# Performance work log

Measured on AMD Instinct MI355X. Metric: run time of the kernel, lower is better.

## Reference

```python
import jax, jax.numpy as jnp
import numpy as np

DIM = 128
HEADS = 4
NS = 7          # neighborhood_size (odd)
RADIUS = NS // 2
EXP = 2         # ffn expansion
EPS = 1e-8


def rmsnorm(x, w):
    # x: [B,C,H,W], w: [1,C,1,1]
    rms = jnp.mean(jnp.square(x), axis=1, keepdims=True)
    return x * jax.lax.rsqrt(rms + EPS) * w


def conv1x1(x, w, b):
    # w: [Cout,Cin], b: [Cout]
    return jnp.einsum('oi,bihw->bohw', w, x) + b[None, :, None, None]


def setup_inputs() -> dict:
    key = jax.random.key(0)
    ks = jax.random.split(key, 20)
    B, C, H, W = 2, DIM, 64, 64
    s = 0.02
    d = {
        'z': jax.random.normal(ks[0], (B, C, H, W), jnp.float32),
        'h': jax.random.normal(ks[1], (B, C, H, W), jnp.float32),
        'wz_norm': jnp.ones((1, C, 1, 1), jnp.float32),
        'wh_norm': jnp.ones((1, C, 1, 1), jnp.float32),
        'wq': jax.random.normal(ks[2], (C, C), jnp.float32) * s,
        'bq': jnp.zeros((C,), jnp.float32),
        'wk': jax.random.normal(ks[3], (C, C), jnp.float32) * s,
        'bk': jnp.zeros((C,), jnp.float32),
        'wv': jax.random.normal(ks[4], (C, C), jnp.float32) * s,
        'bv': jnp.zeros((C,), jnp.float32),
        'wo': jax.random.normal(ks[5], (C, C), jnp.float32) * s,
        'bo': jnp.zeros((C,), jnp.float32),
        'wffn_norm': jnp.ones((1, C, 1, 1), jnp.float32),
        'w1': jax.random.normal(ks[6], (C * EXP, C), jnp.float32) * s,
        'b1': jnp.zeros((C * EXP,), jnp.float32),
        'w2': jax.random.normal(ks[7], (C, C * EXP), jnp.float32) * s,
        'b2': jnp.zeros((C,), jnp.float32),
    }
    return d


def neighborhood_cross_attn(zq, hk, wq, bq, wk, bk, wv, bv, wo, bo):
    B, C, H, W = zq.shape
    hd = C // HEADS
    scale = hd ** (-0.5)
    q = conv1x1(zq, wq, bq)
    k = conv1x1(hk, wk, bk)
    v = conv1x1(hk, wv, bv)
    # [B, heads, H, W, hd]
    qh = q.reshape(B, HEADS, hd, H, W).transpose(0, 1, 3, 4, 2)
    kh = k.reshape(B, HEADS, hd, H, W).transpose(0, 1, 3, 4, 2)
    vh = v.reshape(B, HEADS, hd, H, W).transpose(0, 1, 3, 4, 2)
    offs = jnp.arange(-RADIUS, RADIUS + 1)
    dy, dx = jnp.meshgrid(offs, offs, indexing='ij')
    dy = dy.reshape(-1)  # [K]
    dx = dx.reshape(-1)
    by, bx = jnp.meshgrid(jnp.arange(H), jnp.arange(W), indexing='ij')
    ny = by[:, :, None] + dy  # [H, W, K]
    nx = bx[:, :, None] + dx
    valid = (ny >= 0) & (ny < H) & (nx >= 0) & (nx < W)
    nyc = jnp.clip(ny, 0, H - 1)
    nxc = jnp.clip(nx, 0, W - 1)
    # gather neighbors: [B, heads, H, W, K, hd]
    k_nb = kh[:, :, nyc, nxc]
    v_nb = vh[:, :, nyc, nxc]
    attn = jnp.einsum('bnhwd,bnhwkd->bnhwk', qh, k_nb) * scale
    attn = jnp.where(valid[None, None], attn, jnp.finfo(attn.dtype).min)
    p = jax.nn.softmax(attn, axis=-1)
    out = jnp.einsum('bnhwk,bnhwkd->bnhwd', p, v_nb)
    out = out.transpose(0, 1, 4, 2, 3).reshape(B, C, H, W)
    return conv1x1(out, wo, bo)


def reference(z, h, wz_norm, wh_norm, wq, bq, wk, bk, wv, bv, wo, bo,
              wffn_norm, w1, b1, w2, b2):
    h_norm = rmsnorm(h, wh_norm)
    z_norm = rmsnorm(z, wz_norm)
    z = z + neighborhood_cross_attn(z_norm, h_norm, wq, bq, wk, bk, wv, bv, wo, bo)
    y = rmsnorm(z, wffn_norm)
    y = conv1x1(y, w1, b1)
    y = jax.nn.gelu(y, approximate=False)
    y = conv1x1(y, w2, b2)
    return z + y
```

## Files before the change

kernel.cpp:

```cpp
#include <hip/hip_runtime.h>
#include <math.h>

#define CDIM 128
#define HW   4096
#define HEADS 4
#define HD   32

typedef __attribute__((ext_vector_type(8))) short bf16x8;
typedef __attribute__((ext_vector_type(4))) float f32x4;

static __device__ __forceinline__ unsigned int f2bf(float f) {
  union { float f; unsigned int u; } v; v.f = f;
  unsigned int r = v.u + 0x7FFF + ((v.u >> 16) & 1);
  return r >> 16;
}
static __device__ __forceinline__ float bflo(unsigned int u) {
  return __uint_as_float(u << 16);
}
static __device__ __forceinline__ float bfhi(unsigned int u) {
  return __uint_as_float(u & 0xFFFF0000u);
}
static __device__ __forceinline__ float gelu_f(float v) {
  float y = v * (1.595769122f + 0.071354816f * v * v);
  return v / (1.0f + __expf(-y));
}

__global__ __launch_bounds__(256) void head(
    const float* __restrict__ z, const float* __restrict__ h,
    const float* __restrict__ wzn, const float* __restrict__ whn,
    const float* __restrict__ wq, const float* __restrict__ bq,
    const float* __restrict__ wk, const float* __restrict__ bk,
    const float* __restrict__ wv, const float* __restrict__ bv,
    const float* __restrict__ wo, const float* __restrict__ w1,
    const float* __restrict__ w2, ushort* __restrict__ WB,
    ushort* __restrict__ Qb, ushort* __restrict__ Kb, ushort* __restrict__ Vb) {
  const int sel = blockIdx.y, t = threadIdx.x;
  if (sel == 3) {
    int e = (blockIdx.x * 256 + t) * 4;
    if (e < 81920) {
      const float* src; int off;
      if      (e < 16384) { src = wo; off = 0; }
      else if (e < 49152) { src = w1; off = 16384; }
      else                { src = w2; off = 49152; }
      float4 v = *(const float4*)&src[e - off];
      uint2 r;
      r.x = f2bf(v.x) | (f2bf(v.y) << 16);
      r.y = f2bf(v.z) | (f2bf(v.w) << 16);
      *(uint2*)&WB[49152 + e] = r;
    }
    return;
  }
  __shared__ __align__(16) ushort sW[128 * 128];
  __shared__ __align__(16) ushort sX[64 * 128];
  __shared__ float sh[4][64];

  const float* X    = (sel == 0) ? z : h;
  const float* wn   = (sel == 0) ? wzn : whn;
  const float* Wf   = (sel == 0) ? wq : (sel == 1 ? wk : wv);
  const float* bias = (sel == 0) ? bq : (sel == 1 ? bk : bv);
  ushort* outB      = (sel == 0) ? Qb : (sel == 1 ? Kb : Vb);

#pragma unroll
  for (int i = 0; i < 8; ++i) {
    int u  = t + i * 256;
    int o  = u >> 4;
    int k8 = (u & 15) * 8;
    float4 v0 = *(const float4*)&Wf[o * 128 + k8];
    float4 v1 = *(const float4*)&Wf[o * 128 + k8 + 4];
    uint4 pk;
    pk.x = f2bf(v0.x) | (f2bf(v0.y) << 16);
    pk.y = f2bf(v0.z) | (f2bf(v0.w) << 16);
    pk.z = f2bf(v1.x) | (f2bf(v1.y) << 16);
    pk.w = f2bf(v1.z) | (f2bf(v1.w) << 16);
    int idx = (o * 128 + k8) ^ ((o & 7) << 3);
    *(uint4*)&sW[idx] = pk;
  }

  const int pl = t & 63, g = t >> 6;
  const int gp = blockIdx.x * 64 + pl;
  const size_t xbase = (size_t)(gp >> 12) * CDIM * HW + (gp & 4095);
  float vals[32];
  float ss = 0.f;
#pragma unroll
  for (int j = 0; j < 32; ++j) {
    float v = X[xbase + (size_t)(g * 32 + j) * HW];
    vals[j] = v;
    ss += v * v;
  }
  sh[g][pl] = ss;
  __syncthreads();
  float tot = sh[0][pl] + sh[1][pl] + sh[2][pl] + sh[3][pl];
  float inv = rsqrtf(tot * (1.0f / CDIM) + 1e-8f);
#pragma unroll
  for (int jj = 0; jj < 4; ++jj) {
    unsigned int u[4];
#pragma unroll
    for (int p2 = 0; p2 < 4; ++p2) {
      int j = jj * 8 + p2 * 2;
      float a = vals[j]     * inv * wn[g * 32 + j];
      float b = vals[j + 1] * inv * wn[g * 32 + j + 1];
      u[p2] = f2bf(a) | (f2bf(b) << 16);
    }
    int idx = (pl * 128 + g * 32 + jj * 8) ^ ((pl & 7) << 3);
    *(uint4*)&sX[idx] = make_uint4(u[0], u[1], u[2], u[3]);
  }
  __syncthreads();

  const int w = t >> 6, l = t & 63, lr = l & 15, lk = l >> 4;
  const int m0 = w * 32;
  const int swz = (lr & 7) << 3;
  f32x4 acc[2][4] = {};
#pragma unroll
  for (int k0 = 0; k0 < 128; k0 += 32) {
    bf16x8 a0 = *(const bf16x8*)&sW[((m0 + lr) * 128 + k0 + lk * 8) ^ swz];
    bf16x8 a1 = *(const bf16x8*)&sW[((m0 + 16 + lr) * 128 + k0 + lk * 8) ^ swz];
    bf16x8 b[4];
#pragma unroll
    for (int nf = 0; nf < 4; ++nf)
      b[nf] = *(const bf16x8*)&sX[((nf * 16 + lr) * 128 + k0 + lk * 8) ^ swz];
#pragma unroll
    for (int nf = 0; nf < 4; ++nf) {
      acc[0][nf] = __builtin_amdgcn_mfma_f32_16x16x32_bf16(a0, b[nf], acc[0][nf], 0, 0, 0);
      acc[1][nf] = __builtin_amdgcn_mfma_f32_16x16x32_bf16(a1, b[nf], acc[1][nf], 0, 0, 0);
    }
  }
#pragma unroll
  for (int mf = 0; mf < 2; ++mf) {
    int obase = m0 + mf * 16 + lk * 4;
    f32x4 bv = *(const f32x4*)&bias[obase];
#pragma unroll
    for (int nf = 0; nf < 4; ++nf) {
      int P = blockIdx.x * 64 + nf * 16 + lr;
      uint2 pk;
      pk.x = f2bf(acc[mf][nf][0] + bv[0]) | (f2bf(acc[mf][nf][1] + bv[1]) << 16);
      pk.y = f2bf(acc[mf][nf][2] + bv[2]) | (f2bf(acc[mf][nf][3] + bv[3]) << 16);
      *(uint2*)&outB[(size_t)P * CDIM + obase] = pk;
    }
  }
}

__global__ __launch_bounds__(512) void nattn(
    const ushort* __restrict__ Q, const ushort* __restrict__ K,
    const ushort* __restrict__ V, ushort* __restrict__ ATT) {
  __shared__ __align__(16) unsigned int smem[20480];
  float* sS = (float*)smem;
  const int t  = threadIdx.x;
  const int px = t & 127;
  const int x  = px & 63;
  const int r  = px >> 6;
  const int dg = t >> 7;
  const int y0 = blockIdx.x * 2;
  const int h  = blockIdx.y;
  const int b  = blockIdx.z;
  const int ybase = y0 - 3;

  {
    int yy = t >> 6, xs = t & 63;
    int gy = min(max(ybase + yy, 0), 63);
    size_t gb = ((size_t)(b * HW + gy * 64 + xs)) * 64 + h * 16;
    const unsigned int* Ku = (const unsigned int*)K;
    const unsigned int* Vu = (const unsigned int*)V;
    int lb = (yy * 64 + xs) * 20;
#pragma unroll
    for (int i = 0; i < 4; ++i) {
      uint4 kv = *(const uint4*)&Ku[gb + i * 4];
      uint4 vv = *(const uint4*)&Vu[gb + i * 4];
      *(uint4*)&smem[lb + i * 4]         = kv;
      *(uint4*)&smem[10240 + lb + i * 4] = vv;
    }
  }
  const int Pq = b * HW + (y0 + r) * 64 + x;
  const unsigned int* Qu = (const unsigned int*)Q;
  float q[32];
#pragma unroll
  for (int i = 0; i < 4; ++i) {
    uint4 u4 = *(const uint4*)&Qu[(size_t)Pq * 64 + h * 16 + i * 4];
    q[i*8+0] = bflo(u4.x); q[i*8+1] = bfhi(u4.x);
    q[i*8+2] = bflo(u4.y); q[i*8+3] = bfhi(u4.y);
    q[i*8+4] = bflo(u4.z); q[i*8+5] = bfhi(u4.z);
    q[i*8+6] = bflo(u4.w); q[i*8+7] = bfhi(u4.w);
  }
  __syncthreads();

  const float scale = 0.17677669529663687f;
  const int nb0    = (dg == 0) ? 0 : dg * 12 + 1;
  const int ncount = (dg == 0) ? 13 : 12;
  float sreg[13];
#pragma unroll
  for (int j = 0; j < 13; ++j) {
    if (j < ncount) {
      int nb = nb0 + j;
      int dy = nb / 7 - 3;
      int dx = nb % 7 - 3;
      int ry = r + dy + 3;
      int nx = x + dx;
      int xx = min(max(nx, 0), 63);
      int ny = y0 + r + dy;
      bool valid = (ny >= 0) && (ny <= 63) && (nx >= 0) && (nx <= 63);
      const unsigned int* kb = &smem[(ry * 64 + xx) * 20];
      float acc = 0.f;
#pragma unroll
      for (int c = 0; c < 4; ++c) {
        uint4 u4 = *(const uint4*)&kb[c * 4];
        acc += q[c*8+0] * bflo(u4.x) + q[c*8+1] * bfhi(u4.x);
        acc += q[c*8+2] * bflo(u4.y) + q[c*8+3] * bfhi(u4.y);
        acc += q[c*8+4] * bflo(u4.z) + q[c*8+5] * bfhi(u4.z);
        acc += q[c*8+6] * bflo(u4.w) + q[c*8+7] * bfhi(u4.w);
      }
      sreg[j] = valid ? __expf(acc * scale - 8.0f) : 0.0f;
    }
  }
  __syncthreads();
#pragma unroll
  for (int j = 0; j < 13; ++j)
    if (j < ncount) sS[(nb0 + j) * 128 + px] = sreg[j];
  __syncthreads();

  float o[8] = {0.f, 0.f, 0.f, 0.f, 0.f, 0.f, 0.f, 0.f};
  float sum = 0.f;
#pragma unroll
  for (int nb = 0; nb < 49; ++nb) {
    float p = sS[nb * 128 + px];
    sum += p;
    int ry = r + nb / 7;
    int xx = min(max(x + nb % 7 - 3, 0), 63);
    uint4 u4 = *(const uint4*)&smem[10240 + (ry * 64 + xx) * 20 + dg * 4];
    o[0] += p * bflo(u4.x); o[1] += p * bfhi(u4.x);
    o[2] += p * bflo(u4.y); o[3] += p * bfhi(u4.y);
    o[4] += p * bflo(u4.z); o[5] += p * bfhi(u4.z);
    o[6] += p * bflo(u4.w); o[7] += p * bfhi(u4.w);
  }
  float inv = 1.0f / sum;
  unsigned int pk[4];
#pragma unroll
  for (int j = 0; j < 4; ++j)
    pk[j] = f2bf(o[2*j] * inv) | (f2bf(o[2*j+1] * inv) << 16);
  *(uint4*)&ATT[(size_t)Pq * CDIM + h * HD + dg * 8] = make_uint4(pk[0], pk[1], pk[2], pk[3]);
}

__global__ __launch_bounds__(256) void tail(
    const ushort* __restrict__ ATT, const ushort* __restrict__ WB,
    const float* __restrict__ bo, const float* __restrict__ z,
    const float* __restrict__ wfn, const float* __restrict__ b1,
    const float* __restrict__ b2, float* __restrict__ out) {
  __shared__ __align__(16) float  zlds[32][132];
  __shared__ __align__(16) ushort fn_s[32 * 128];
  __shared__ __align__(16) ushort hid_s[32 * 256];
  __shared__ float sums[32][17];
  __shared__ float sinv[32];
  const ushort* Wo = WB + 49152;
  const ushort* W1 = WB + 65536;
  const ushort* W2 = WB + 98304;
  const int t = threadIdx.x, w = t >> 6, l = t & 63, lr = l & 15, lk = l >> 4;
  const int pblk = blockIdx.x * 32;
  const int m0 = w * 32;

  {
    const ushort* A0 = Wo + (size_t)(m0 + lr) * 128 + lk * 8;
    const ushort* A1 = A0 + 16 * 128;
    const ushort* B0 = ATT + (size_t)(pblk + lr) * 128 + lk * 8;
    const ushort* B1 = B0 + 16 * 128;
    f32x4 acc[2][2] = {};
#pragma unroll
    for (int k0 = 0; k0 < 128; k0 += 32) {
      bf16x8 a0 = *(const bf16x8*)(A0 + k0);
      bf16x8 a1 = *(const bf16x8*)(A1 + k0);
      bf16x8 b0 = *(const bf16x8*)(B0 + k0);
      bf16x8 b1 = *(const bf16x8*)(B1 + k0);
      acc[0][0] = __builtin_amdgcn_mfma_f32_16x16x32_bf16(a0, b0, acc[0][0], 0, 0, 0);
      acc[0][1] = __builtin_amdgcn_mfma_f32_16x16x32_bf16(a0, b1, acc[0][1], 0, 0, 0);
      acc[1][0] = __builtin_amdgcn_mfma_f32_16x16x32_bf16(a1, b0, acc[1][0], 0, 0, 0);
      acc[1][1] = __builtin_amdgcn_mfma_f32_16x16x32_bf16(a1, b1, acc[1][1], 0, 0, 0);
    }
#pragma unroll
    for (int nf = 0; nf < 2; ++nf) {
      int px = nf * 16 + lr;
      int P  = pblk + px;
      int b_ = P >> 12, p = P & 4095;
      float ss = 0.f;
#pragma unroll
      for (int mf = 0; mf < 2; ++mf) {
        int row0 = m0 + mf * 16 + lk * 4;
        f32x4 bv = *(const f32x4*)&bo[row0];
        f32x4 rr;
#pragma unroll
        for (int j = 0; j < 4; ++j) {
          size_t gi = ((size_t)(b_ * CDIM + row0 + j)) * HW + p;
          float u = acc[mf][nf][j] + bv[j] + z[gi];
          rr[j] = u;
          ss += u * u;
        }
        *(f32x4*)&zlds[px][row0] = rr;
      }
      sums[px][w * 4 + lk] = ss;
    }
  }
  __syncthreads();
  if (t < 32) {
    float tot = 0.f;
#pragma unroll
    for (int i = 0; i < 16; ++i) tot += sums[t][i];
    sinv[t] = rsqrtf(tot * (1.0f / CDIM) + 1e-8f);
  }
  __syncthreads();
#pragma unroll
  for (int nf = 0; nf < 2; ++nf) {
    int px = nf * 16 + lr;
    float inv = sinv[px];
#pragma unroll
    for (int mf = 0; mf < 2; ++mf) {
      int row0 = m0 + mf * 16 + lk * 4;
      f32x4 uu = *(const f32x4*)&zlds[px][row0];
      f32x4 wf = *(const f32x4*)&wfn[row0];
      uint2 pk;
      pk.x = f2bf(uu[0] * inv * wf[0]) | (f2bf(uu[1] * inv * wf[1]) << 16);
      pk.y = f2bf(uu[2] * inv * wf[2]) | (f2bf(uu[3] * inv * wf[3]) << 16);
      int idx = (px * 128 + row0) ^ ((px & 7) << 3);
      *(uint2*)&fn_s[idx] = pk;
    }
  }
  __syncthreads();
  {
    const int hm0 = w * 64;
    const ushort* A0 = W1 + (size_t)(hm0 + lr) * 128 + lk * 8;
    f32x4 acc1[4][2] = {};
#pragma unroll
    for (int k0 = 0; k0 < 128; k0 += 32) {
      bf16x8 a[4], b[2];
#pragma unroll
      for (int mf = 0; mf < 4; ++mf) a[mf] = *(const bf16x8*)(A0 + mf * 16 * 128 + k0);
#pragma unroll
      for (int nf = 0; nf < 2; ++nf) {
        int px = nf * 16 + lr;
        b[nf] = *(const bf16x8*)&fn_s[(px * 128 + k0 + lk * 8) ^ ((px & 7) << 3)];
      }
#pragma unroll
      for (int mf = 0; mf < 4; ++mf)
#pragma unroll
        for (int nf = 0; nf < 2; ++nf)
          acc1[mf][nf] = __builtin_amdgcn_mfma_f32_16x16x32_bf16(a[mf], b[nf], acc1[mf][nf], 0, 0, 0);
    }
#pragma unroll
    for (int mf = 0; mf < 4; ++mf) {
      int ch0 = hm0 + mf * 16 + lk * 4;
      f32x4 bv = *(const f32x4*)&b1[ch0];
#pragma unroll
      for (int nf = 0; nf < 2; ++nf) {
        int px = nf * 16 + lr;
        float v0 = gelu_f(acc1[mf][nf][0] + bv[0]);
        float v1 = gelu_f(acc1[mf][nf][1] + bv[1]);
        float v2 = gelu_f(acc1[mf][nf][2] + bv[2]);
        float v3 = gelu_f(acc1[mf][nf][3] + bv[3]);
        uint2 pk;
        pk.x = f2bf(v0) | (f2bf(v1) << 16);
        pk.y = f2bf(v2) | (f2bf(v3) << 16);
        int idx = (px * 256 + ch0) ^ ((px & 7) << 3);
        *(uint2*)&hid_s[idx] = pk;
      }
    }
  }
  __syncthreads();
  {
    const ushort* C0 = W2 + (size_t)(m0 + lr) * 256 + lk * 8;
    f32x4 acc2[2][2] = {};
#pragma unroll
    for (int k0 = 0; k0 < 256; k0 += 32) {
      bf16x8 a0 = *(const bf16x8*)(C0 + k0);
      bf16x8 a1 = *(const bf16x8*)(C0 + 16 * 256 + k0);
      bf16x8 b[2];
#pragma unroll
      for (int nf = 0; nf < 2; ++nf) {
        int px = nf * 16 + lr;
        b[nf] = *(const bf16x8*)&hid_s[(px * 256 + k0 + lk * 8) ^ ((px & 7) << 3)];
      }
      acc2[0][0] = __builtin_amdgcn_mfma_f32_16x16x32_bf16(a0, b[0], acc2[0][0], 0, 0, 0);
      acc2[0][1] = __builtin_amdgcn_mfma_f32_16x16x32_bf16(a0, b[1], acc2[0][1], 0, 0, 0);
      acc2[1][0] = __builtin_amdgcn_mfma_f32_16x16x32_bf16(a1, b[0], acc2[1][0], 0, 0, 0);
      acc2[1][1] = __builtin_amdgcn_mfma_f32_16x16x32_bf16(a1, b[1], acc2[1][1], 0, 0, 0);
    }
#pragma unroll
    for (int mf = 0; mf < 2; ++mf) {
      int row0 = m0 + mf * 16 + lk * 4;
      f32x4 bv = *(const f32x4*)&b2[row0];
#pragma unroll
      for (int nf = 0; nf < 2; ++nf) {
        int px = nf * 16 + lr;
        int P  = pblk + px;
        int b_ = P >> 12, p = P & 4095;
        f32x4 zz = *(const f32x4*)&zlds[px][row0];
#pragma unroll
        for (int j = 0; j < 4; ++j) {
          size_t gi = ((size_t)(b_ * CDIM + row0 + j)) * HW + p;
          out[gi] = acc2[mf][nf][j] + bv[j] + zz[j];
        }
      }
    }
  }
}

extern "C" void kernel_launch(void* const* d_in, const int* in_sizes, int n_in,
                              void* d_out, int out_size, void* d_ws, size_t ws_size,
                              hipStream_t stream) {
  const float* z   = (const float*)d_in[0];
  const float* h   = (const float*)d_in[1];
  const float* wzn = (const float*)d_in[2];
  const float* whn = (const float*)d_in[3];
  const float* wq  = (const float*)d_in[4];
  const float* bq  = (const float*)d_in[5];
  const float* wk  = (const float*)d_in[6];
  const float* bk  = (const float*)d_in[7];
  const float* wv  = (const float*)d_in[8];
  const float* bv  = (const float*)d_in[9];
  const float* wo  = (const float*)d_in[10];
  const float* bo  = (const float*)d_in[11];
  const float* wfn = (const float*)d_in[12];
  const float* w1  = (const float*)d_in[13];
  const float* b1  = (const float*)d_in[14];
  const float* w2  = (const float*)d_in[15];
  const float* b2  = (const float*)d_in[16];
  float* out = (float*)d_out;

  const size_t U = 1048576;
  ushort* Qb  = (ushort*)d_ws;
  ushort* Kb  = Qb + U;
  ushort* Vb  = Kb + U;
  ushort* ATT = Vb + U;
  ushort* WB  = ATT + U;

  head<<<dim3(128, 4), 256, 0, stream>>>(z, h, wzn, whn, wq, bq, wk, bk, wv, bv,
                                         wo, w1, w2, WB, Qb, Kb, Vb);
  nattn<<<dim3(32, HEADS, 2), 512, 0, stream>>>(Qb, Kb, Vb, ATT);
  tail<<<dim3(256), 256, 0, stream>>>(ATT, WB, bo, z, wfn, b1, b2, out);
}
```

Before: 38.64 us.

## Process one row per attention block and pack softmax weights as bf16 pairs

The neighborhood attention kernel now handles a single output row per block with 256 threads instead of two rows with 512, doubling the grid and shrinking the K/V halo tile from 8 to 7 rows. Softmax numerators are stored as packed bf16 pairs in shared memory, which cuts LDS usage and read traffic for the weighted-V pass. Single-row blocks give up the halo reuse between adjacent rows, so total K/V global loads rise. The bf16 rounding of the probabilities adds precision loss to the output.

```diff
diff --git a/kernel.cpp b/kernel.cpp
--- a/kernel.cpp
+++ b/kernel.cpp
@@ -139,37 +139,39 @@
   }
 }
 
-__global__ __launch_bounds__(512) void nattn(
+__global__ __launch_bounds__(256) void nattn(
     const ushort* __restrict__ Q, const ushort* __restrict__ K,
     const ushort* __restrict__ V, ushort* __restrict__ ATT) {
-  __shared__ __align__(16) unsigned int smem[20480];
-  float* sS = (float*)smem;
+  __shared__ __align__(16) unsigned int smem[17920];
   const int t  = threadIdx.x;
-  const int px = t & 127;
-  const int x  = px & 63;
-  const int r  = px >> 6;
-  const int dg = t >> 7;
-  const int y0 = blockIdx.x * 2;
+  const int x  = t & 63;
+  const int dg = t >> 6;
+  const int y  = blockIdx.x;
   const int h  = blockIdx.y;
   const int b  = blockIdx.z;
-  const int ybase = y0 - 3;
 
   {
-    int yy = t >> 6, xs = t & 63;
-    int gy = min(max(ybase + yy, 0), 63);
-    size_t gb = ((size_t)(b * HW + gy * 64 + xs)) * 64 + h * 16;
     const unsigned int* Ku = (const unsigned int*)K;
     const unsigned int* Vu = (const unsigned int*)V;
-    int lb = (yy * 64 + xs) * 20;
-#pragma unroll
-    for (int i = 0; i < 4; ++i) {
-      uint4 kv = *(const uint4*)&Ku[gb + i * 4];
-      uint4 vv = *(const uint4*)&Vu[gb + i * 4];
-      *(uint4*)&smem[lb + i * 4]         = kv;
-      *(uint4*)&smem[10240 + lb + i * 4] = vv;
-    }
-  }
-  const int Pq = b * HW + (y0 + r) * 64 + x;
+#pragma unroll
+    for (int i = 0; i < 2; ++i) {
+      int pp = t + i * 256;
+      if (pp < 448) {
+        int ry = pp >> 6, xs = pp & 63;
+        int gy = min(max(y - 3 + ry, 0), 63);
+        size_t gb = ((size_t)(b * HW + gy * 64 + xs)) * 64 + h * 16;
+        int lb = pp * 20;
+#pragma unroll
+        for (int c = 0; c < 4; ++c) {
+          uint4 kv = *(const uint4*)&Ku[gb + c * 4];
+          uint4 vv = *(const uint4*)&Vu[gb + c * 4];
+          *(uint4*)&smem[lb + c * 4]        = kv;
+          *(uint4*)&smem[8960 + lb + c * 4] = vv;
+        }
+      }
+    }
+  }
+  const int Pq = b * HW + y * 64 + x;
   const unsigned int* Qu = (const unsigned int*)Q;
   float q[32];
 #pragma unroll
@@ -192,10 +194,10 @@
       int nb = nb0 + j;
       int dy = nb / 7 - 3;
       int dx = nb % 7 - 3;
-      int ry = r + dy + 3;
+      int ry = dy + 3;
+      int ny = y + dy;
       int nx = x + dx;
       int xx = min(max(nx, 0), 63);
-      int ny = y0 + r + dy;
       bool valid = (ny >= 0) && (ny <= 63) && (nx >= 0) && (nx <= 63);
       const unsigned int* kb = &smem[(ry * 64 + xx) * 20];
       float acc = 0.f;
@@ -211,24 +213,45 @@
     }
   }
   __syncthreads();
-#pragma unroll
-  for (int j = 0; j < 13; ++j)
-    if (j < ncount) sS[(nb0 + j) * 128 + px] = sreg[j];
+  {
+    int wbase  = (dg == 0) ? 0 : 7 + (dg - 1) * 6;
+    int npairs = (dg == 0) ? 7 : 6;
+#pragma unroll
+    for (int j = 0; j < 7; ++j) {
+      if (j < npairs) {
+        float p0 = sreg[2 * j];
+        float p1 = (2 * j + 1 < ncount) ? sreg[2 * j + 1] : 0.f;
+        smem[(wbase + j) * 64 + x] = f2bf(p0) | (f2bf(p1) << 16);
+      }
+    }
+  }
   __syncthreads();
 
   float o[8] = {0.f, 0.f, 0.f, 0.f, 0.f, 0.f, 0.f, 0.f};
   float sum = 0.f;
 #pragma unroll
-  for (int nb = 0; nb < 49; ++nb) {
-    float p = sS[nb * 128 + px];
-    sum += p;
-    int ry = r + nb / 7;
-    int xx = min(max(x + nb % 7 - 3, 0), 63);
-    uint4 u4 = *(const uint4*)&smem[10240 + (ry * 64 + xx) * 20 + dg * 4];
-    o[0] += p * bflo(u4.x); o[1] += p * bfhi(u4.x);
-    o[2] += p * bflo(u4.y); o[3] += p * bfhi(u4.y);
-    o[4] += p * bflo(u4.z); o[5] += p * bfhi(u4.z);
-    o[6] += p * bflo(u4.w); o[7] += p * bfhi(u4.w);
+  for (int wdx = 0; wdx < 25; ++wdx) {
+    unsigned int pw = smem[wdx * 64 + x];
+    int base_nb, cnt;
+    if (wdx < 7)       { base_nb = 2 * wdx;           cnt = (wdx == 6) ? 1 : 2; }
+    else if (wdx < 13) { base_nb = 13 + 2 * (wdx - 7);  cnt = 2; }
+    else if (wdx < 19) { base_nb = 25 + 2 * (wdx - 13); cnt = 2; }
+    else               { base_nb = 37 + 2 * (wdx - 19); cnt = 2; }
+#pragma unroll
+    for (int hh = 0; hh < 2; ++hh) {
+      if (hh < cnt) {
+        int nb = base_nb + hh;
+        float p = hh ? bfhi(pw) : bflo(pw);
+        sum += p;
+        int ry = nb / 7;
+        int xx = min(max(x + nb % 7 - 3, 0), 63);
+        uint4 u4 = *(const uint4*)&smem[8960 + (ry * 64 + xx) * 20 + dg * 4];
+        o[0] += p * bflo(u4.x); o[1] += p * bfhi(u4.x);
+        o[2] += p * bflo(u4.y); o[3] += p * bfhi(u4.y);
+        o[4] += p * bflo(u4.z); o[5] += p * bfhi(u4.z);
+        o[6] += p * bflo(u4.w); o[7] += p * bfhi(u4.w);
+      }
+    }
   }
   float inv = 1.0f / sum;
   unsigned int pk[4];
@@ -429,6 +452,6 @@
 
   head<<<dim3(128, 4), 256, 0, stream>>>(z, h, wzn, whn, wq, bq, wk, bk, wv, bv,
                                          wo, w1, w2, WB, Qb, Kb, Vb);
-  nattn<<<dim3(32, HEADS, 2), 512, 0, stream>>>(Qb, Kb, Vb, ATT);
+  nattn<<<dim3(64, HEADS, 2), 256, 0, stream>>>(Qb, Kb, Vb, ATT);
   tail<<<dim3(256), 256, 0, stream>>>(ATT, WB, bo, z, wfn, b1, b2, out);
 }
```

New measurement: 40.26 us. 1.04x slower.
